# Optimization experiments

Measured on AMD Instinct MI355X. Metric: run time of the kernel, lower is better.

## Reference

```python
import jax, jax.numpy as jnp
import numpy as np

B, S, D, E, K = 4, 2048, 1024, 8, 2
EPS, W_THRES, TEMP = 1e-4, 0.1, 1.0


def setup_inputs() -> dict:
    key = jax.random.key(0)
    k1, k2, k3, k4, k5 = jax.random.split(key, 5)
    x = jax.random.normal(k1, (B, S, D), dtype=jnp.float32)
    gate_W = jax.random.normal(k2, (D, E), dtype=jnp.float32) * 0.02
    gate_b = jnp.zeros((E,), dtype=jnp.float32)
    expert_W = jax.random.normal(k3, (E, D, D), dtype=jnp.float32) * 0.02
    expert_b = jnp.zeros((E, D), dtype=jnp.float32)
    return {"x": x, "gate_W": gate_W, "gate_b": gate_b,
            "expert_W": expert_W, "expert_b": expert_b}


def reference(x, gate_W, gate_b, expert_W, expert_b):
    # Gating: linear -> temperature -> clamp-min(eps) -> softmax
    scores = jnp.maximum((x @ gate_W + gate_b) / TEMP, EPS)      # [B,S,E]
    p = jax.nn.softmax(scores, axis=-1)                           # [B,S,E]
    _, topk_idx = jax.lax.top_k(p, K)                             # [B,S,K]
    # boolean membership mask of selected experts
    topk_mask = jax.nn.one_hot(topk_idx, E, dtype=p.dtype).sum(-2) > 0  # [B,S,E]
    # weights: clamp-min(weight_thres), normalized by detached sum over selected
    w = jnp.maximum(p, W_THRES)                                   # [B,S,E]
    w_gather = jnp.take_along_axis(w, topk_idx, axis=-1)          # [B,S,K]
    total = jax.lax.stop_gradient(w_gather.sum(-1, keepdims=True))
    w = w / total
    comb = jnp.where(topk_mask, w, jnp.zeros_like(w))             # [B,S,E]
    # Dense equivalent of gather/expert/scatter loop (E small): each expert
    # is Linear(D, D); masked combine weights zero out unselected experts.
    y = jnp.einsum('bsd,edf->bsef', x, expert_W) + expert_b       # [B,S,E,D]
    out = jnp.einsum('bsef,bse->bsf', y, comb) / K                # [B,S,D]
    return out
```

## Files before the change

kernel.cpp:

```cpp
#include <hip/hip_runtime.h>
#include <hip/hip_fp16.h>
#include <stdint.h>

#define TOK 8192
#define DIM 1024
#define NE 8
#define NT 72
#define NCT 4

typedef short bf16x8 __attribute__((ext_vector_type(8)));
typedef float f32x4 __attribute__((ext_vector_type(4)));

__device__ __forceinline__ unsigned short f2bf(float f) {
  unsigned int u = __float_as_uint(f);
  u += 0x7FFFu + ((u >> 16) & 1u);
  return (unsigned short)(u >> 16);
}

__device__ __forceinline__ void gl_lds16(const void* g, void* l) {
  __builtin_amdgcn_global_load_lds(
      (__attribute__((address_space(1))) unsigned int*)(g),
      (__attribute__((address_space(3))) unsigned int*)(l), 16, 0, 0);
}

__device__ __forceinline__ unsigned lds_off(const void* p) {
  return (unsigned)(size_t)(__attribute__((address_space(3))) const void*)p;
}

__global__ __launch_bounds__(256) void gate_transpose(
    const float* __restrict__ x, const float* __restrict__ gW,
    const float* __restrict__ gb, unsigned short* __restrict__ xb,
    int* __restrict__ eSel, float* __restrict__ wSel, int* __restrict__ cnt,
    const float* __restrict__ W, unsigned short* __restrict__ Wt)
{
  __shared__ __align__(16) float smem[NE * DIM];

  if (blockIdx.x >= 2048) {
    float (*t2)[65] = (float(*)[65])smem;
    const int b  = blockIdx.x - 2048;
    const int e  = b >> 8;
    const int db = (b >> 4) & 15;
    const int fb = b & 15;
    const int d0 = db * 64, f0 = fb * 64;
    const int tid = threadIdx.x;
#pragma unroll
    for (int h = 0; h < 4; ++h) {
      const int idx = tid + h * 256;
      const int r = idx >> 4, c4 = idx & 15;
      float4 v = *(const float4*)&W[((size_t)e * DIM + d0 + r) * DIM + f0 + c4 * 4];
      t2[r][c4 * 4 + 0] = v.x;
      t2[r][c4 * 4 + 1] = v.y;
      t2[r][c4 * 4 + 2] = v.z;
      t2[r][c4 * 4 + 3] = v.w;
    }
    __syncthreads();
#pragma unroll
    for (int h = 0; h < 8; ++h) {
      const int o = tid + h * 256;
      const int f = o >> 5, k2 = (o & 31) * 2;
      const unsigned int lo = f2bf(t2[k2][f]);
      const unsigned int hi = f2bf(t2[k2 + 1][f]);
      *(unsigned int*)&Wt[((size_t)e * DIM + f0 + f) * DIM + d0 + k2] =
          lo | (hi << 16);
    }
    return;
  }

  if (blockIdx.x == 0 && threadIdx.x < NE) cnt[threadIdx.x] = 0;

  float* gWs = smem;
#pragma unroll
  for (int h = 0; h < 8; ++h) {
    const int m = threadIdx.x + h * 256;
    float4 v = ((const float4*)gW)[m];
    const int d = m >> 1, e0 = (m & 1) * 4;
    gWs[(e0 + 0) * DIM + d] = v.x;
    gWs[(e0 + 1) * DIM + d] = v.y;
    gWs[(e0 + 2) * DIM + d] = v.z;
    gWs[(e0 + 3) * DIM + d] = v.w;
  }
  __syncthreads();

  const int wave = threadIdx.x >> 6;
  const int lane = threadIdx.x & 63;
  const int t = blockIdx.x * 4 + wave;
  const float4* xrow = (const float4*)(x + (size_t)t * DIM);
  ushort4* xbrow = (ushort4*)(xb + (size_t)t * DIM);

  double acc[NE];
#pragma unroll
  for (int e = 0; e < NE; ++e) acc[e] = 0.0;

#pragma unroll
  for (int i = 0; i < 4; ++i) {
    const int j = i * 64 + lane;
    float4 v = xrow[j];
    ushort4 pk;
    pk.x = f2bf(v.x); pk.y = f2bf(v.y); pk.z = f2bf(v.z); pk.w = f2bf(v.w);
    xbrow[j] = pk;
#pragma unroll
    for (int e = 0; e < NE; ++e) {
      float4 gv = *(const float4*)&gWs[e * DIM + j * 4];
      acc[e] += (double)v.x * (double)gv.x + (double)v.y * (double)gv.y
              + (double)v.z * (double)gv.z + (double)v.w * (double)gv.w;
    }
  }
#pragma unroll
  for (int off = 32; off > 0; off >>= 1) {
#pragma unroll
    for (int e = 0; e < NE; ++e)
      acc[e] += __shfl_xor(acc[e], off, 64);
  }

  if (lane == 0) {
    double s[NE];
#pragma unroll
    for (int e = 0; e < NE; ++e) {
      s[e] = acc[e] + (double)gb[e];
      if (s[e] < 1e-4) s[e] = 1e-4;
    }
    int e0 = 0;
    for (int e = 1; e < NE; ++e) if (s[e] > s[e0]) e0 = e;
    int e1 = (e0 == 0) ? 1 : 0;
    for (int e = 0; e < NE; ++e) if (e != e0 && s[e] > s[e1]) e1 = e;
    float m = (float)s[e0];
    float Z = 0.f, pf[NE];
#pragma unroll
    for (int e = 0; e < NE; ++e) { pf[e] = __expf((float)s[e] - m); Z += pf[e]; }
    float w0 = pf[e0] / Z; if (w0 < 0.1f) w0 = 0.1f;
    float w1 = pf[e1] / Z; if (w1 < 0.1f) w1 = 0.1f;
    const float inv = 0.5f / (w0 + w1);
    eSel[t * 2 + 0] = e0;
    eSel[t * 2 + 1] = e1;
    wSel[t * 2 + 0] = w0 * inv;
    wSel[t * 2 + 1] = w1 * inv;
  }
}

__global__ __launch_bounds__(256) void scatter_kernel(
    const int* __restrict__ eSel, const float* __restrict__ wSel,
    int* __restrict__ cnt, int* __restrict__ listTok, float* __restrict__ listW)
{
  __shared__ int lcnt[NE];
  __shared__ int base[NE];
  const int tid = threadIdx.x;
  if (tid < NE) lcnt[tid] = 0;
  __syncthreads();

  const int t = blockIdx.x * 256 + tid;
  const int e0 = eSel[t * 2 + 0];
  const int e1 = eSel[t * 2 + 1];
  const float w0 = wSel[t * 2 + 0];
  const float w1 = wSel[t * 2 + 1];
  const int l0 = atomicAdd(&lcnt[e0], 1);
  const int l1 = atomicAdd(&lcnt[e1], 1);
  __syncthreads();
  if (tid < NE) base[tid] = atomicAdd(&cnt[tid], lcnt[tid]);
  __syncthreads();

  const int p0 = base[e0] + l0;
  listTok[e0 * TOK + p0] = t * 2 + 0;
  listW [e0 * TOK + p0] = w0;
  const int p1 = base[e1] + l1;
  listTok[e1 * TOK + p1] = t * 2 + 1;
  listW [e1 * TOK + p1] = w1;
}

#define WAITVM(n) asm volatile("s_waitcnt vmcnt(" #n ")" ::: "memory")

#define STG(kt, bs)                                                          \
  { const int off_ = (kt) * 32;                                              \
    gl_lds16(srcA0 + off_, &As[bs][w * 512]);                                \
    gl_lds16(srcA1 + off_, &As[bs][128 * 32 + w * 512]);                     \
    gl_lds16(srcB0 + off_, &Bs[bs][w * 512]);                                \
    gl_lds16(srcB1 + off_, &Bs[bs][128 * 32 + w * 512]); }

#define CMP(bs)                                                              \
  { const unsigned aA = asOff + (unsigned)(bs) * 16384u + rdA2;              \
    const unsigned bA = bsOff + (unsigned)(bs) * 16384u + rdB2;              \
    bf16x8 a0,a1,a2,a3,a4,a5,a6,a7,b0,b1,b2,b3;                              \
    asm volatile(                                                            \
      "ds_read_b128 %0, %12 offset:0\n\t"                                    \
      "ds_read_b128 %1, %12 offset:1024\n\t"                                 \
      "ds_read_b128 %2, %12 offset:2048\n\t"                                 \
      "ds_read_b128 %3, %12 offset:3072\n\t"                                 \
      "ds_read_b128 %8, %13 offset:0\n\t"                                    \
      "ds_read_b128 %9, %13 offset:1024\n\t"                                 \
      "ds_read_b128 %10, %13 offset:2048\n\t"                                \
      "ds_read_b128 %11, %13 offset:3072\n\t"                                \
      "ds_read_b128 %4, %12 offset:4096\n\t"                                 \
      "ds_read_b128 %5, %12 offset:5120\n\t"                                 \
      "ds_read_b128 %6, %12 offset:6144\n\t"                                 \
      "ds_read_b128 %7, %12 offset:7168\n\t"                                 \
      "s_waitcnt lgkmcnt(4)"                                                 \
      : "=&v"(a0),"=&v"(a1),"=&v"(a2),"=&v"(a3),                             \
        "=&v"(a4),"=&v"(a5),"=&v"(a6),"=&v"(a7),                             \
        "=&v"(b0),"=&v"(b1),"=&v"(b2),"=&v"(b3)                              \
      : "v"(aA), "v"(bA)                                                     \
      : "memory");                                                           \
    __builtin_amdgcn_sched_barrier(0);                                       \
    bf16x8 afL[4] = {a0, a1, a2, a3};                                        \
    bf16x8 afH[4] = {a4, a5, a6, a7};                                        \
    bf16x8 bfr[4] = {b0, b1, b2, b3};                                        \
    __builtin_amdgcn_s_setprio(1);                                           \
    _Pragma("unroll")                                                        \
    for (int mt = 0; mt < 4; ++mt)                                           \
      _Pragma("unroll")                                                      \
      for (int nt = 0; nt < 4; ++nt)                                         \
        acc[mt][nt] = __builtin_amdgcn_mfma_f32_16x16x32_bf16(               \
            afL[mt], bfr[nt], acc[mt][nt], 0, 0, 0);                         \
    __builtin_amdgcn_s_setprio(0);                                           \
    asm volatile("s_waitcnt lgkmcnt(0)" ::: "memory");                       \
    __builtin_amdgcn_sched_barrier(0);                                       \
    __builtin_amdgcn_s_setprio(1);                                           \
    _Pragma("unroll")                                                        \
    for (int mt = 0; mt < 4; ++mt)                                           \
      _Pragma("unroll")                                                      \
      for (int nt = 0; nt < 4; ++nt)                                         \
        acc[mt + 4][nt] = __builtin_amdgcn_mfma_f32_16x16x32_bf16(           \
            afH[mt], bfr[nt], acc[mt + 4][nt], 0, 0, 0);                     \
    __builtin_amdgcn_s_setprio(0); }

__global__ __launch_bounds__(512, 2) void moe_gemm(
    const unsigned short* __restrict__ xb, const unsigned short* __restrict__ Wt,
    const float* __restrict__ eb, const int* __restrict__ cnt,
    const int* __restrict__ listTok, const float* __restrict__ listW,
    __half* __restrict__ yslot)
{
  const int dId = blockIdx.x % NT;
  const int cT  = blockIdx.x / NT;
  int e = -1, r0 = 0, rows = 0, accT = 0;
#pragma unroll
  for (int ee = 0; ee < NE; ++ee) {
    const int c = cnt[ee];
    const int nt = (c + 255) >> 8;
    if (dId >= accT && dId < accT + nt) {
      e = ee; r0 = (dId - accT) * 256;
      rows = c - r0; if (rows > 256) rows = 256;
    }
    accT += nt;
  }
  if (e < 0) return;

  __shared__ __align__(16) unsigned short As[3][256 * 32];
  __shared__ __align__(16) unsigned short Bs[3][256 * 32];
  __shared__ int   tid_s[256];
  __shared__ float w_s[256];

  const int tid = threadIdx.x;
  if (tid < 256) {
    if (tid < rows) {
      tid_s[tid] = listTok[e * TOK + r0 + tid];
      w_s[tid]   = listW [e * TOK + r0 + tid];
    } else {
      tid_s[tid] = 0;
      w_s[tid]   = 0.0f;
    }
  }
  __syncthreads();

  const int w    = tid >> 6;
  const int lane = tid & 63;
  const int qsrc = (lane & 3) ^ ((lane >> 3) & 3);
  const int lr   = lane >> 2;
  const unsigned short* srcA0 = xb + (size_t)(tid_s[      w * 16 + lr] >> 1) * DIM + qsrc * 8;
  const unsigned short* srcA1 = xb + (size_t)(tid_s[128 + w * 16 + lr] >> 1) * DIM + qsrc * 8;
  const size_t bbase = ((size_t)e * DIM + cT * 256) * DIM;
  const unsigned short* srcB0 = Wt + bbase + (size_t)(      w * 16 + lr) * DIM + qsrc * 8;
  const unsigned short* srcB1 = Wt + bbase + (size_t)(128 + w * 16 + lr) * DIM + qsrc * 8;

  const int wr = w >> 2, wc = w & 3;
  const int mrow = lane & 15;
  const int qg   = lane >> 4;
  const int s8   = (qg ^ ((mrow >> 1) & 3)) * 8;
  const unsigned rdA2 = (unsigned)(((wr * 128 + mrow) * 32 + s8) * 2);
  const unsigned rdB2 = (unsigned)(((wc * 64 + mrow) * 32 + s8) * 2);
  const unsigned asOff = lds_off(&As[0][0]);
  const unsigned bsOff = lds_off(&Bs[0][0]);

  f32x4 acc[8][4];
#pragma unroll
  for (int i = 0; i < 8; ++i)
#pragma unroll
    for (int j = 0; j < 4; ++j)
      acc[i][j] = {0.f, 0.f, 0.f, 0.f};

  STG(0, 0);
  STG(1, 1);
  WAITVM(4);
  __builtin_amdgcn_s_barrier();

  int sC = 0, sS = 2;
#pragma unroll 1
  for (int kt = 0; kt < 32; ++kt) {
    if (kt < 30) STG(kt + 2, sS);
    CMP(sC);
    if (kt < 30) {
      WAITVM(4);
      __builtin_amdgcn_s_barrier();
    } else if (kt == 30) {
      WAITVM(0);
      __builtin_amdgcn_s_barrier();
    }
    sC = (sC == 2) ? 0 : sC + 1;
    sS = (sS == 2) ? 0 : sS + 1;
  }

  const int colBase = cT * 256 + wc * 64 + mrow;
  float bias[4];
#pragma unroll
  for (int nt = 0; nt < 4; ++nt)
    bias[nt] = eb[(size_t)e * DIM + colBase + nt * 16];
#pragma unroll
  for (int mt = 0; mt < 8; ++mt) {
#pragma unroll
    for (int r = 0; r < 4; ++r) {
      const int rloc = wr * 128 + mt * 16 + (lane >> 4) * 4 + r;
      if (rloc < rows) {
        const int tk    = tid_s[rloc];
        const float wgt = w_s[rloc];
        __half* dst = yslot + ((size_t)(tk & 1) * TOK + (size_t)(tk >> 1)) * DIM;
#pragma unroll
        for (int nt = 0; nt < 4; ++nt)
          dst[colBase + nt * 16] = __float2half(wgt * (acc[mt][nt][r] + bias[nt]));
      }
    }
  }
}

__global__ __launch_bounds__(256) void combine(
    const __half* __restrict__ y0, const __half* __restrict__ y1,
    float4* __restrict__ out)
{
  const size_t i = (size_t)blockIdx.x * 256 + threadIdx.x;
  const ushort4 ua = ((const ushort4*)y0)[i];
  const ushort4 ub = ((const ushort4*)y1)[i];
  const __half* ah = (const __half*)&ua;
  const __half* bh = (const __half*)&ub;
  float4 o;
  o.x = __half2float(ah[0]) + __half2float(bh[0]);
  o.y = __half2float(ah[1]) + __half2float(bh[1]);
  o.z = __half2float(ah[2]) + __half2float(bh[2]);
  o.w = __half2float(ah[3]) + __half2float(bh[3]);
  out[i] = o;
}

extern "C" void kernel_launch(void* const* d_in, const int* in_sizes, int n_in,
                              void* d_out, int out_size, void* d_ws, size_t ws_size,
                              hipStream_t stream)
{
  const float* x  = (const float*)d_in[0];
  const float* gW = (const float*)d_in[1];
  const float* gb = (const float*)d_in[2];
  const float* eW = (const float*)d_in[3];
  const float* eb = (const float*)d_in[4];
  float* out = (float*)d_out;

  char* p = (char*)d_ws;
  unsigned short* xb = (unsigned short*)p;  p += (size_t)TOK * DIM * 2;
  unsigned short* Wt = (unsigned short*)p;  p += (size_t)NE * DIM * DIM * 2;
  __half* yslot = (__half*)p;               p += (size_t)2 * TOK * DIM * 2;
  int* cnt = (int*)p;                       p += 256;
  int* listTok = (int*)p;                   p += (size_t)NE * TOK * 4;
  float* listW = (float*)p;                 p += (size_t)NE * TOK * 4;

  int*   eSel = (int*)yslot;
  float* wSel = (float*)((char*)yslot + TOK * 8);

  gate_transpose<<<4096, 256, 0, stream>>>(x, gW, gb, xb, eSel, wSel, cnt, eW, Wt);
  scatter_kernel<<<TOK / 256, 256, 0, stream>>>(eSel, wSel, cnt, listTok, listW);
  moe_gemm<<<NT * NCT, 512, 0, stream>>>(xb, Wt, eb, cnt, listTok, listW, yslot);
  combine<<<TOK * DIM / 4 / 256, 256, 0, stream>>>(
      yslot, yslot + (size_t)TOK * DIM, (float4*)out);
}
```

Before: 199.8 us.

## Fuse combine into GEMM via atomic adds and double-buffer LDS fragment reads

```diff
diff --git a/kernel.cpp b/kernel.cpp
--- a/kernel.cpp
+++ b/kernel.cpp
@@ -31,9 +31,19 @@
     const float* __restrict__ x, const float* __restrict__ gW,
     const float* __restrict__ gb, unsigned short* __restrict__ xb,
     int* __restrict__ eSel, float* __restrict__ wSel, int* __restrict__ cnt,
-    const float* __restrict__ W, unsigned short* __restrict__ Wt)
+    const float* __restrict__ W, unsigned short* __restrict__ Wt,
+    float4* __restrict__ outz)
 {
   __shared__ __align__(16) float smem[NE * DIM];
+
+  if (blockIdx.x >= 4096) {
+    const float4 z = {0.f, 0.f, 0.f, 0.f};
+    const unsigned base = (blockIdx.x - 4096) * 256 + threadIdx.x;
+#pragma unroll
+    for (int h = 0; h < 4; ++h)
+      outz[base + h * 524288] = z;
+    return;
+  }
 
   if (blockIdx.x >= 2048) {
     float (*t2)[65] = (float(*)[65])smem;
@@ -167,6 +177,8 @@
 }
 
 #define WAITVM(n) asm volatile("s_waitcnt vmcnt(" #n ")" ::: "memory")
+#define WAITLGKM  { asm volatile("s_waitcnt lgkmcnt(0)" ::: "memory"); \
+                    __builtin_amdgcn_sched_barrier(0); }
 
 #define STG(kt, bs)                                                          \
   { const int off_ = (kt) * 32;                                              \
@@ -175,57 +187,48 @@
     gl_lds16(srcB0 + off_, &Bs[bs][w * 512]);                                \
     gl_lds16(srcB1 + off_, &Bs[bs][128 * 32 + w * 512]); }
 
-#define CMP(bs)                                                              \
+#define RD(P, bs)                                                            \
   { const unsigned aA = asOff + (unsigned)(bs) * 16384u + rdA2;              \
     const unsigned bA = bsOff + (unsigned)(bs) * 16384u + rdB2;              \
-    bf16x8 a0,a1,a2,a3,a4,a5,a6,a7,b0,b1,b2,b3;                              \
     asm volatile(                                                            \
       "ds_read_b128 %0, %12 offset:0\n\t"                                    \
       "ds_read_b128 %1, %12 offset:1024\n\t"                                 \
       "ds_read_b128 %2, %12 offset:2048\n\t"                                 \
       "ds_read_b128 %3, %12 offset:3072\n\t"                                 \
-      "ds_read_b128 %8, %13 offset:0\n\t"                                    \
-      "ds_read_b128 %9, %13 offset:1024\n\t"                                 \
-      "ds_read_b128 %10, %13 offset:2048\n\t"                                \
-      "ds_read_b128 %11, %13 offset:3072\n\t"                                \
       "ds_read_b128 %4, %12 offset:4096\n\t"                                 \
       "ds_read_b128 %5, %12 offset:5120\n\t"                                 \
       "ds_read_b128 %6, %12 offset:6144\n\t"                                 \
       "ds_read_b128 %7, %12 offset:7168\n\t"                                 \
-      "s_waitcnt lgkmcnt(4)"                                                 \
-      : "=&v"(a0),"=&v"(a1),"=&v"(a2),"=&v"(a3),                             \
-        "=&v"(a4),"=&v"(a5),"=&v"(a6),"=&v"(a7),                             \
-        "=&v"(b0),"=&v"(b1),"=&v"(b2),"=&v"(b3)                              \
+      "ds_read_b128 %8, %13 offset:0\n\t"                                    \
+      "ds_read_b128 %9, %13 offset:1024\n\t"                                 \
+      "ds_read_b128 %10, %13 offset:2048\n\t"                                \
+      "ds_read_b128 %11, %13 offset:3072"                                    \
+      : "=&v"(P##a0),"=&v"(P##a1),"=&v"(P##a2),"=&v"(P##a3),                 \
+        "=&v"(P##a4),"=&v"(P##a5),"=&v"(P##a6),"=&v"(P##a7),                 \
+        "=&v"(P##b0),"=&v"(P##b1),"=&v"(P##b2),"=&v"(P##b3)                  \
       : "v"(aA), "v"(bA)                                                     \
       : "memory");                                                           \
-    __builtin_amdgcn_sched_barrier(0);                                       \
-    bf16x8 afL[4] = {a0, a1, a2, a3};                                        \
-    bf16x8 afH[4] = {a4, a5, a6, a7};                                        \
-    bf16x8 bfr[4] = {b0, b1, b2, b3};                                        \
+    __builtin_amdgcn_sched_barrier(0); }
+
+#define MM(P)                                                                \
+  { bf16x8 af[8] = {P##a0, P##a1, P##a2, P##a3, P##a4, P##a5, P##a6, P##a7}; \
+    bf16x8 bfv[4] = {P##b0, P##b1, P##b2, P##b3};                            \
     __builtin_amdgcn_s_setprio(1);                                           \
     _Pragma("unroll")                                                        \
-    for (int mt = 0; mt < 4; ++mt)                                           \
+    for (int mt = 0; mt < 8; ++mt)                                           \
       _Pragma("unroll")                                                      \
       for (int nt = 0; nt < 4; ++nt)                                         \
         acc[mt][nt] = __builtin_amdgcn_mfma_f32_16x16x32_bf16(               \
-            afL[mt], bfr[nt], acc[mt][nt], 0, 0, 0);                         \
-    __builtin_amdgcn_s_setprio(0);                                           \
-    asm volatile("s_waitcnt lgkmcnt(0)" ::: "memory");                       \
-    __builtin_amdgcn_sched_barrier(0);                                       \
-    __builtin_amdgcn_s_setprio(1);                                           \
-    _Pragma("unroll")                                                        \
-    for (int mt = 0; mt < 4; ++mt)                                           \
-      _Pragma("unroll")                                                      \
-      for (int nt = 0; nt < 4; ++nt)                                         \
-        acc[mt + 4][nt] = __builtin_amdgcn_mfma_f32_16x16x32_bf16(           \
-            afH[mt], bfr[nt], acc[mt + 4][nt], 0, 0, 0);                     \
+            af[mt], bfv[nt], acc[mt][nt], 0, 0, 0);                          \
     __builtin_amdgcn_s_setprio(0); }
+
+#define BAR __builtin_amdgcn_s_barrier()
 
 __global__ __launch_bounds__(512, 2) void moe_gemm(
     const unsigned short* __restrict__ xb, const unsigned short* __restrict__ Wt,
     const float* __restrict__ eb, const int* __restrict__ cnt,
     const int* __restrict__ listTok, const float* __restrict__ listW,
-    __half* __restrict__ yslot)
+    float* __restrict__ out)
 {
   const int dId = blockIdx.x % NT;
   const int cT  = blockIdx.x / NT;
@@ -242,8 +245,8 @@
   }
   if (e < 0) return;
 
-  __shared__ __align__(16) unsigned short As[3][256 * 32];
-  __shared__ __align__(16) unsigned short Bs[3][256 * 32];
+  __shared__ __align__(16) unsigned short As[4][256 * 32];
+  __shared__ __align__(16) unsigned short Bs[4][256 * 32];
   __shared__ int   tid_s[256];
   __shared__ float w_s[256];
 
@@ -285,26 +288,27 @@
     for (int j = 0; j < 4; ++j)
       acc[i][j] = {0.f, 0.f, 0.f, 0.f};
 
-  STG(0, 0);
-  STG(1, 1);
+  bf16x8 Ea0,Ea1,Ea2,Ea3,Ea4,Ea5,Ea6,Ea7,Eb0,Eb1,Eb2,Eb3;
+  bf16x8 Oa0,Oa1,Oa2,Oa3,Oa4,Oa5,Oa6,Oa7,Ob0,Ob1,Ob2,Ob3;
+
+  STG(0, 0); STG(1, 1); STG(2, 2);
   WAITVM(4);
-  __builtin_amdgcn_s_barrier();
-
-  int sC = 0, sS = 2;
+  BAR;
+  RD(E, 0);
+  WAITLGKM;
+
 #pragma unroll 1
-  for (int kt = 0; kt < 32; ++kt) {
-    if (kt < 30) STG(kt + 2, sS);
-    CMP(sC);
-    if (kt < 30) {
-      WAITVM(4);
-      __builtin_amdgcn_s_barrier();
-    } else if (kt == 30) {
-      WAITVM(0);
-      __builtin_amdgcn_s_barrier();
-    }
-    sC = (sC == 2) ? 0 : sC + 1;
-    sS = (sS == 2) ? 0 : sS + 1;
-  }
+  for (int t = 0; t < 7; ++t) {
+    const int k4 = t * 4;
+    STG(k4 + 3, 3); RD(O, 1); MM(E); WAITLGKM; WAITVM(4); BAR;
+    STG(k4 + 4, 0); RD(E, 2); MM(O); WAITLGKM; WAITVM(4); BAR;
+    STG(k4 + 5, 1); RD(O, 3); MM(E); WAITLGKM; WAITVM(4); BAR;
+    STG(k4 + 6, 2); RD(E, 0); MM(O); WAITLGKM; WAITVM(4); BAR;
+  }
+  STG(31, 3); RD(O, 1); MM(E); WAITLGKM; WAITVM(4); BAR;
+  RD(E, 2); MM(O); WAITLGKM; WAITVM(0); BAR;
+  RD(O, 3); MM(E); WAITLGKM;
+  MM(O);
 
   const int colBase = cT * 256 + wc * 64 + mrow;
   float bias[4];
@@ -319,30 +323,14 @@
       if (rloc < rows) {
         const int tk    = tid_s[rloc];
         const float wgt = w_s[rloc];
-        __half* dst = yslot + ((size_t)(tk & 1) * TOK + (size_t)(tk >> 1)) * DIM;
+        float* dst = out + (size_t)(tk >> 1) * DIM;
 #pragma unroll
         for (int nt = 0; nt < 4; ++nt)
-          dst[colBase + nt * 16] = __float2half(wgt * (acc[mt][nt][r] + bias[nt]));
+          unsafeAtomicAdd(&dst[colBase + nt * 16],
+                          wgt * (acc[mt][nt][r] + bias[nt]));
       }
     }
   }
-}
-
-__global__ __launch_bounds__(256) void combine(
-    const __half* __restrict__ y0, const __half* __restrict__ y1,
-    float4* __restrict__ out)
-{
-  const size_t i = (size_t)blockIdx.x * 256 + threadIdx.x;
-  const ushort4 ua = ((const ushort4*)y0)[i];
-  const ushort4 ub = ((const ushort4*)y1)[i];
-  const __half* ah = (const __half*)&ua;
-  const __half* bh = (const __half*)&ub;
-  float4 o;
-  o.x = __half2float(ah[0]) + __half2float(bh[0]);
-  o.y = __half2float(ah[1]) + __half2float(bh[1]);
-  o.z = __half2float(ah[2]) + __half2float(bh[2]);
-  o.w = __half2float(ah[3]) + __half2float(bh[3]);
-  out[i] = o;
 }
 
 extern "C" void kernel_launch(void* const* d_in, const int* in_sizes, int n_in,
@@ -359,17 +347,16 @@
   char* p = (char*)d_ws;
   unsigned short* xb = (unsigned short*)p;  p += (size_t)TOK * DIM * 2;
   unsigned short* Wt = (unsigned short*)p;  p += (size_t)NE * DIM * DIM * 2;
-  __half* yslot = (__half*)p;               p += (size_t)2 * TOK * DIM * 2;
+  char* scratch = p;                        p += (size_t)2 * TOK * DIM * 2;
   int* cnt = (int*)p;                       p += 256;
   int* listTok = (int*)p;                   p += (size_t)NE * TOK * 4;
   float* listW = (float*)p;                 p += (size_t)NE * TOK * 4;
 
-  int*   eSel = (int*)yslot;
-  float* wSel = (float*)((char*)yslot + TOK * 8);
-
-  gate_transpose<<<4096, 256, 0, stream>>>(x, gW, gb, xb, eSel, wSel, cnt, eW, Wt);
+  int*   eSel = (int*)scratch;
+  float* wSel = (float*)(scratch + TOK * 8);
+
+  gate_transpose<<<6144, 256, 0, stream>>>(x, gW, gb, xb, eSel, wSel, cnt,
+                                           eW, Wt, (float4*)out);
   scatter_kernel<<<TOK / 256, 256, 0, stream>>>(eSel, wSel, cnt, listTok, listW);
-  moe_gemm<<<NT * NCT, 512, 0, stream>>>(xb, Wt, eb, cnt, listTok, listW, yslot);
-  combine<<<TOK * DIM / 4 / 256, 256, 0, stream>>>(
-      yslot, yslot + (size_t)TOK * DIM, (float4*)out);
-}
+  moe_gemm<<<NT * NCT, 512, 0, stream>>>(xb, Wt, eb, cnt, listTok, listW, out);
+}
```

Measured after the change: 252.7 us. 26.5% more time.
